# Kernel optimization log

Measured on AMD Instinct MI355X. Metric: run time of the kernel, lower is better.

Reference implementation:

```python
import jax, jax.numpy as jnp
import numpy as np

P = 0.1  # channel error probability (init kwarg error_prob)


def _binary_entropy(p):
    # matches tensor_binary_entropy: clamp log2 at dtype min
    q = 1.0 - p
    min_real = jnp.finfo(jnp.float32).min
    l2p = jnp.maximum(jnp.log2(p), min_real)
    l2q = jnp.maximum(jnp.log2(q), min_real)
    return -p * l2p - q * l2q


def setup_inputs() -> dict:
    key = jax.random.key(0)
    k1, k2, k3, k4 = jax.random.split(key, 4)
    B, L, V = 128, 64, 4096
    logits = jax.random.normal(k1, (B, L, V), jnp.float32)
    probs = jax.nn.softmax(logits, axis=-1)          # relaxed one-hot probs
    entropy = jax.random.uniform(k2, (B, L), jnp.float32)
    rand_mask = jax.random.uniform(k3, (B, L), jnp.float32)
    replacement_ids = jax.random.randint(k4, (B, L), 0, V - 2)
    return {"probs": probs, "entropy": entropy,
            "rand_mask": rand_mask, "replacement_ids": replacement_ids}


def reference(probs, entropy, rand_mask, replacement_ids):
    # SymmetricChannel.gs, training branch, fully vectorized / predicated.
    B, L, V = probs.shape
    mask = rand_mask < P                                  # [B,L] target positions
    any_hit = mask.any()                                  # torch early-returns if sum()==0

    # torch: replaced_probs[:, replacement_symbols] = 1 - eos  -> every masked row
    # is written at EVERY column appearing among the masked replacement ids.
    col_hit = jnp.zeros((V,), bool).at[replacement_ids.reshape(-1)].max(mask.reshape(-1))

    eos = probs[..., :1]                                  # [B,L,1] original EOS prob
    col = jnp.arange(V)
    base = jnp.where(col == 0, eos, jnp.zeros_like(eos))  # replaced_probs[:,0]=eos
    replaced = jnp.where(col_hit, 1.0 - eos, base)        # [B,L,V]

    probs_out = jnp.where(mask[..., None] & any_hit, replaced, probs)

    # torch adds H_b(p) + log2(probs.size(1) - 2)  (size(1) == max_len, kept faithfully)
    delta = _binary_entropy(jnp.float32(P)) + jnp.log2(jnp.float32(L - 2))
    entropy_out = jnp.where(any_hit, entropy + delta, entropy)
    return probs_out, entropy_out
```

## Files before the change

### kernel.cpp

```cpp
#include <hip/hip_runtime.h>


#define V_DIM   4096
#define N_ROWS  8192
#define P_CONST 0.1f
#define DELTA_CONST 6.4231919039761563f

typedef float f32x4 __attribute__((ext_vector_type(4)));

__global__ __launch_bounds__(256)
void sc_fused_kernel(const f32x4* __restrict__ probs4,
                     const float* __restrict__ probs_s,
                     const f32x4* __restrict__ rand4,
                     const float* __restrict__ rand_s,
                     const int*   __restrict__ repl,
                     const float* __restrict__ entropy,
                     f32x4*       __restrict__ out4,
                     float*       __restrict__ entropy_out)
{
    __shared__ unsigned colhit[V_DIM / 32];
    __shared__ unsigned anyflag;
    const int t   = threadIdx.x;
    const int bid = blockIdx.x;

    if (bid < N_ROWS) {
        const int  row      = bid;
        const long rowbase4 = (long)row * (V_DIM / 4);
        const bool m        = rand_s[row] < P_CONST;

        if (m) {
            if (t < V_DIM / 32) colhit[t] = 0u;
            __syncthreads();
            #pragma unroll
            for (int k = 0; k < N_ROWS / 4 / 256; ++k) {
                const int   i4 = t + k * 256;
                const f32x4 r  = rand4[i4];
                const int   i0 = i4 * 4;
                if (r.x < P_CONST) { const int id = repl[i0    ]; atomicOr(&colhit[id >> 5], 1u << (id & 31)); }
                if (r.y < P_CONST) { const int id = repl[i0 + 1]; atomicOr(&colhit[id >> 5], 1u << (id & 31)); }
                if (r.z < P_CONST) { const int id = repl[i0 + 2]; atomicOr(&colhit[id >> 5], 1u << (id & 31)); }
                if (r.w < P_CONST) { const int id = repl[i0 + 3]; atomicOr(&colhit[id >> 5], 1u << (id & 31)); }
            }
            __syncthreads();

            const float eos = probs_s[(long)row * V_DIM];
            const float om  = 1.0f - eos;
            #pragma unroll
            for (int k = 0; k < 4; ++k) {
                const int      c4 = t + k * 256;
                const unsigned w  = colhit[c4 >> 3];
                const int      c0 = c4 * 4;
                f32x4 r;
                r.x = ((w >> ( c0      & 31)) & 1u) ? om : ((c0 == 0) ? eos : 0.0f);
                r.y = ((w >> ((c0 + 1) & 31)) & 1u) ? om : 0.0f;
                r.z = ((w >> ((c0 + 2) & 31)) & 1u) ? om : 0.0f;
                r.w = ((w >> ((c0 + 3) & 31)) & 1u) ? om : 0.0f;
                __builtin_nontemporal_store(r, &out4[rowbase4 + c4]);
            }
        } else {
            #pragma unroll
            for (int k = 0; k < 4; ++k) {
                const int   c4 = t + k * 256;
                const f32x4 v  = __builtin_nontemporal_load(&probs4[rowbase4 + c4]);
                __builtin_nontemporal_store(v, &out4[rowbase4 + c4]);
            }
        }
    } else {
        const int eb = bid - N_ROWS;
        if (t == 0) anyflag = 0u;
        __syncthreads();
        bool la = false;
        #pragma unroll
        for (int k = 0; k < N_ROWS / 4 / 256; ++k) {
            const f32x4 r = rand4[t + k * 256];
            la = la || (r.x < P_CONST) || (r.y < P_CONST) ||
                       (r.z < P_CONST) || (r.w < P_CONST);
        }
        if (la) atomicOr(&anyflag, 1u);
        __syncthreads();
        const float d = anyflag ? DELTA_CONST : 0.0f;
        const int   i = eb * 256 + t;
        entropy_out[i] = entropy[i] + d;
    }
}

extern "C" void kernel_launch(void* const* d_in, const int* in_sizes, int n_in,
                              void* d_out, int out_size, void* d_ws, size_t ws_size,
                              hipStream_t stream)
{
    const float* probs     = (const float*)d_in[0];
    const float* entropy   = (const float*)d_in[1];
    const float* rand_mask = (const float*)d_in[2];
    const int*   repl      = (const int*)  d_in[3];

    float* out         = (float*)d_out;
    float* probs_out   = out;
    float* entropy_out = out + (long)N_ROWS * V_DIM;

    sc_fused_kernel<<<N_ROWS + 32, 256, 0, stream>>>(
        (const f32x4*)probs, probs,
        (const f32x4*)rand_mask, rand_mask,
        repl, entropy,
        (f32x4*)probs_out, entropy_out);
}
```

Measured before the change: 50.39 us.

## Hoist column-hit bitmap into single-block prefix kernel, process two rows per block

Adds a single-block prefix kernel that builds the column-hit bitmap and the any-hit flag once, writes the bitmap to workspace, and updates entropy. Before, every masked row's block rescanned all 8192 mask/replacement entries. The main kernel then processes two rows per block and copies the small bitmap from global memory only when a row is masked. This removes the redundant per-row scans in exchange for a second kernel launch and a serial dependency on a tiny one-block kernel.

```diff
diff --git a/kernel.cpp b/kernel.cpp
--- a/kernel.cpp
+++ b/kernel.cpp
@@ -2,85 +2,116 @@
 
 
 #define V_DIM   4096
+#define V4      (V_DIM / 4)
 #define N_ROWS  8192
 #define P_CONST 0.1f
 #define DELTA_CONST 6.4231919039761563f
 
 typedef float f32x4 __attribute__((ext_vector_type(4)));
 
-__global__ __launch_bounds__(256)
-void sc_fused_kernel(const f32x4* __restrict__ probs4,
-                     const float* __restrict__ probs_s,
-                     const f32x4* __restrict__ rand4,
-                     const float* __restrict__ rand_s,
-                     const int*   __restrict__ repl,
-                     const float* __restrict__ entropy,
-                     f32x4*       __restrict__ out4,
-                     float*       __restrict__ entropy_out)
+__global__ __launch_bounds__(1024)
+void sc_prefix_kernel(const f32x4* __restrict__ rand4,
+                      const int4*  __restrict__ repl4,
+                      const f32x4* __restrict__ entropy4,
+                      unsigned*    __restrict__ colhit_out,
+                      f32x4*       __restrict__ entropy_out4)
 {
     __shared__ unsigned colhit[V_DIM / 32];
     __shared__ unsigned anyflag;
-    const int t   = threadIdx.x;
-    const int bid = blockIdx.x;
+    const int t = threadIdx.x;
+    if (t < V_DIM / 32) colhit[t] = 0u;
+    if (t == 0) anyflag = 0u;
+    __syncthreads();
 
-    if (bid < N_ROWS) {
-        const int  row      = bid;
-        const long rowbase4 = (long)row * (V_DIM / 4);
-        const bool m        = rand_s[row] < P_CONST;
+    const f32x4 r0 = rand4[t], r1 = rand4[t + 1024];
+    const int4  q0 = repl4[t], q1 = repl4[t + 1024];
 
-        if (m) {
-            if (t < V_DIM / 32) colhit[t] = 0u;
-            __syncthreads();
-            #pragma unroll
-            for (int k = 0; k < N_ROWS / 4 / 256; ++k) {
-                const int   i4 = t + k * 256;
-                const f32x4 r  = rand4[i4];
-                const int   i0 = i4 * 4;
-                if (r.x < P_CONST) { const int id = repl[i0    ]; atomicOr(&colhit[id >> 5], 1u << (id & 31)); }
-                if (r.y < P_CONST) { const int id = repl[i0 + 1]; atomicOr(&colhit[id >> 5], 1u << (id & 31)); }
-                if (r.z < P_CONST) { const int id = repl[i0 + 2]; atomicOr(&colhit[id >> 5], 1u << (id & 31)); }
-                if (r.w < P_CONST) { const int id = repl[i0 + 3]; atomicOr(&colhit[id >> 5], 1u << (id & 31)); }
-            }
-            __syncthreads();
+    bool any = false;
+    {
+        if (r0.x < P_CONST) { any = true; atomicOr(&colhit[q0.x >> 5], 1u << (q0.x & 31)); }
+        if (r0.y < P_CONST) { any = true; atomicOr(&colhit[q0.y >> 5], 1u << (q0.y & 31)); }
+        if (r0.z < P_CONST) { any = true; atomicOr(&colhit[q0.z >> 5], 1u << (q0.z & 31)); }
+        if (r0.w < P_CONST) { any = true; atomicOr(&colhit[q0.w >> 5], 1u << (q0.w & 31)); }
+        if (r1.x < P_CONST) { any = true; atomicOr(&colhit[q1.x >> 5], 1u << (q1.x & 31)); }
+        if (r1.y < P_CONST) { any = true; atomicOr(&colhit[q1.y >> 5], 1u << (q1.y & 31)); }
+        if (r1.z < P_CONST) { any = true; atomicOr(&colhit[q1.z >> 5], 1u << (q1.z & 31)); }
+        if (r1.w < P_CONST) { any = true; atomicOr(&colhit[q1.w >> 5], 1u << (q1.w & 31)); }
+    }
+    if (any) atomicOr(&anyflag, 1u);
+    __syncthreads();
 
-            const float eos = probs_s[(long)row * V_DIM];
-            const float om  = 1.0f - eos;
-            #pragma unroll
-            for (int k = 0; k < 4; ++k) {
-                const int      c4 = t + k * 256;
-                const unsigned w  = colhit[c4 >> 3];
-                const int      c0 = c4 * 4;
-                f32x4 r;
-                r.x = ((w >> ( c0      & 31)) & 1u) ? om : ((c0 == 0) ? eos : 0.0f);
-                r.y = ((w >> ((c0 + 1) & 31)) & 1u) ? om : 0.0f;
-                r.z = ((w >> ((c0 + 2) & 31)) & 1u) ? om : 0.0f;
-                r.w = ((w >> ((c0 + 3) & 31)) & 1u) ? om : 0.0f;
-                __builtin_nontemporal_store(r, &out4[rowbase4 + c4]);
-            }
-        } else {
-            #pragma unroll
-            for (int k = 0; k < 4; ++k) {
-                const int   c4 = t + k * 256;
-                const f32x4 v  = __builtin_nontemporal_load(&probs4[rowbase4 + c4]);
-                __builtin_nontemporal_store(v, &out4[rowbase4 + c4]);
-            }
+    if (t < V_DIM / 32) colhit_out[t] = colhit[t];
+
+    const float d = anyflag ? DELTA_CONST : 0.0f;
+    f32x4 e0 = entropy4[t], e1 = entropy4[t + 1024];
+    e0.x += d; e0.y += d; e0.z += d; e0.w += d;
+    e1.x += d; e1.y += d; e1.z += d; e1.w += d;
+    entropy_out4[t]        = e0;
+    entropy_out4[t + 1024] = e1;
+}
+
+__device__ __forceinline__ void synth_row(const unsigned* colhit, float eos,
+                                          long rowbase4, int t,
+                                          f32x4* __restrict__ out4)
+{
+    const float om = 1.0f - eos;
+    #pragma unroll
+    for (int k = 0; k < 4; ++k) {
+        const int      c4 = t + k * 256;
+        const unsigned w  = colhit[c4 >> 3];
+        const int      c0 = c4 * 4;
+        f32x4 r;
+        r.x = ((w >> ( c0      & 31)) & 1u) ? om : ((c0 == 0) ? eos : 0.0f);
+        r.y = ((w >> ((c0 + 1) & 31)) & 1u) ? om : 0.0f;
+        r.z = ((w >> ((c0 + 2) & 31)) & 1u) ? om : 0.0f;
+        r.w = ((w >> ((c0 + 3) & 31)) & 1u) ? om : 0.0f;
+        __builtin_nontemporal_store(r, &out4[rowbase4 + c4]);
+    }
+}
+
+__global__ __launch_bounds__(256)
+void sc_main_kernel(const f32x4*    __restrict__ probs4,
+                    const float*    __restrict__ probs_s,
+                    const float*    __restrict__ rand_s,
+                    const unsigned* __restrict__ colhit_g,
+                    f32x4*          __restrict__ out4)
+{
+    __shared__ unsigned colhit[V_DIM / 32];
+    const int  t     = threadIdx.x;
+    const int  row0  = blockIdx.x * 2;
+    const bool m0    = rand_s[row0]     < P_CONST;
+    const bool m1    = rand_s[row0 + 1] < P_CONST;
+    const long base4 = (long)row0 * V4;
+
+    if (!m0 && !m1) {
+        #pragma unroll
+        for (int k = 0; k < 8; ++k) {
+            const f32x4 v = probs4[base4 + t + k * 256];
+            __builtin_nontemporal_store(v, &out4[base4 + t + k * 256]);
         }
+        return;
+    }
+
+    if (t < V_DIM / 32) colhit[t] = colhit_g[t];
+    __syncthreads();
+
+    if (m0) {
+        synth_row(colhit, probs_s[(long)row0 * V_DIM], base4, t, out4);
     } else {
-        const int eb = bid - N_ROWS;
-        if (t == 0) anyflag = 0u;
-        __syncthreads();
-        bool la = false;
         #pragma unroll
-        for (int k = 0; k < N_ROWS / 4 / 256; ++k) {
-            const f32x4 r = rand4[t + k * 256];
-            la = la || (r.x < P_CONST) || (r.y < P_CONST) ||
-                       (r.z < P_CONST) || (r.w < P_CONST);
+        for (int k = 0; k < 4; ++k) {
+            const f32x4 v = probs4[base4 + t + k * 256];
+            __builtin_nontemporal_store(v, &out4[base4 + t + k * 256]);
         }
-        if (la) atomicOr(&anyflag, 1u);
-        __syncthreads();
-        const float d = anyflag ? DELTA_CONST : 0.0f;
-        const int   i = eb * 256 + t;
-        entropy_out[i] = entropy[i] + d;
+    }
+    if (m1) {
+        synth_row(colhit, probs_s[(long)(row0 + 1) * V_DIM], base4 + V4, t, out4);
+    } else {
+        #pragma unroll
+        for (int k = 0; k < 4; ++k) {
+            const f32x4 v = probs4[base4 + V4 + t + k * 256];
+            __builtin_nontemporal_store(v, &out4[base4 + V4 + t + k * 256]);
+        }
     }
 }
 
@@ -93,13 +124,15 @@
     const float* rand_mask = (const float*)d_in[2];
     const int*   repl      = (const int*)  d_in[3];
 
-    float* out         = (float*)d_out;
-    float* probs_out   = out;
-    float* entropy_out = out + (long)N_ROWS * V_DIM;
+    float*    out         = (float*)d_out;
+    float*    probs_out   = out;
+    float*    entropy_out = out + (long)N_ROWS * V_DIM;
+    unsigned* colhit_ws   = (unsigned*)d_ws;
 
-    sc_fused_kernel<<<N_ROWS + 32, 256, 0, stream>>>(
-        (const f32x4*)probs, probs,
-        (const f32x4*)rand_mask, rand_mask,
-        repl, entropy,
-        (f32x4*)probs_out, entropy_out);
+    sc_prefix_kernel<<<1, 1024, 0, stream>>>(
+        (const f32x4*)rand_mask, (const int4*)repl,
+        (const f32x4*)entropy, colhit_ws, (f32x4*)entropy_out);
+
+    sc_main_kernel<<<N_ROWS / 2, 256, 0, stream>>>(
+        (const f32x4*)probs, probs, rand_mask, colhit_ws, (f32x4*)probs_out);
 }
```

Result: faster. 47.55 us (-5.6%).

## Build column bitmap once per writer block and split copy from synthesis

Applied to the files above, without the earlier changes.

Before, every masked row's block rebuilt the full column-hit bitmap by scanning all 8192 mask entries. Now 256 dedicated writer blocks each build the bitmap once and synthesize the masked rows in their 32-row slice. The entropy update is folded into those same writer blocks. Copy blocks now handle two rows each and only copy unmasked rows, with vectorized int4 loads of the replacement ids. The trade-off is that writer blocks loop serially over their rows, which can cause load imbalance.

```diff
diff --git a/kernel.cpp b/kernel.cpp
--- a/kernel.cpp
+++ b/kernel.cpp
@@ -2,85 +2,106 @@
 
 
 #define V_DIM   4096
+#define V4      (V_DIM / 4)
 #define N_ROWS  8192
+#define NWRITER 256
+#define WROWS   (N_ROWS / NWRITER)
 #define P_CONST 0.1f
 #define DELTA_CONST 6.4231919039761563f
 
 typedef float f32x4 __attribute__((ext_vector_type(4)));
 
+__device__ __forceinline__ void synth_row(const unsigned* colhit, float eos,
+                                          long rowbase4, int t,
+                                          f32x4* __restrict__ out4)
+{
+    const float om = 1.0f - eos;
+    #pragma unroll
+    for (int k = 0; k < 4; ++k) {
+        const int      c4 = t + k * 256;
+        const unsigned w  = colhit[c4 >> 3];
+        const int      c0 = c4 * 4;
+        f32x4 r;
+        r.x = ((w >> ( c0      & 31)) & 1u) ? om : ((c0 == 0) ? eos : 0.0f);
+        r.y = ((w >> ((c0 + 1) & 31)) & 1u) ? om : 0.0f;
+        r.z = ((w >> ((c0 + 2) & 31)) & 1u) ? om : 0.0f;
+        r.w = ((w >> ((c0 + 3) & 31)) & 1u) ? om : 0.0f;
+        __builtin_nontemporal_store(r, &out4[rowbase4 + c4]);
+    }
+}
+
 __global__ __launch_bounds__(256)
-void sc_fused_kernel(const f32x4* __restrict__ probs4,
-                     const float* __restrict__ probs_s,
-                     const f32x4* __restrict__ rand4,
-                     const float* __restrict__ rand_s,
-                     const int*   __restrict__ repl,
-                     const float* __restrict__ entropy,
-                     f32x4*       __restrict__ out4,
-                     float*       __restrict__ entropy_out)
+void sc_onekernel(const f32x4* __restrict__ probs4,
+                  const float* __restrict__ probs_s,
+                  const f32x4* __restrict__ rand4,
+                  const float* __restrict__ rand_s,
+                  const int4*  __restrict__ repl4,
+                  const float* __restrict__ entropy,
+                  f32x4*       __restrict__ out4,
+                  float*       __restrict__ entropy_out)
 {
-    __shared__ unsigned colhit[V_DIM / 32];
-    __shared__ unsigned anyflag;
     const int t   = threadIdx.x;
     const int bid = blockIdx.x;
 
-    if (bid < N_ROWS) {
-        const int  row      = bid;
-        const long rowbase4 = (long)row * (V_DIM / 4);
-        const bool m        = rand_s[row] < P_CONST;
+    if (bid < NWRITER) {
+        __shared__ unsigned colhit[V_DIM / 32];
+        __shared__ unsigned anyflag;
+        if (t < V_DIM / 32) colhit[t] = 0u;
+        if (t == 0) anyflag = 0u;
+        __syncthreads();
 
-        if (m) {
-            if (t < V_DIM / 32) colhit[t] = 0u;
-            __syncthreads();
-            #pragma unroll
-            for (int k = 0; k < N_ROWS / 4 / 256; ++k) {
-                const int   i4 = t + k * 256;
-                const f32x4 r  = rand4[i4];
-                const int   i0 = i4 * 4;
-                if (r.x < P_CONST) { const int id = repl[i0    ]; atomicOr(&colhit[id >> 5], 1u << (id & 31)); }
-                if (r.y < P_CONST) { const int id = repl[i0 + 1]; atomicOr(&colhit[id >> 5], 1u << (id & 31)); }
-                if (r.z < P_CONST) { const int id = repl[i0 + 2]; atomicOr(&colhit[id >> 5], 1u << (id & 31)); }
-                if (r.w < P_CONST) { const int id = repl[i0 + 3]; atomicOr(&colhit[id >> 5], 1u << (id & 31)); }
-            }
-            __syncthreads();
+        bool any = false;
+        #pragma unroll
+        for (int k = 0; k < N_ROWS / 4 / 256; ++k) {
+            const int   i4 = t + k * 256;
+            const f32x4 r  = rand4[i4];
+            const int4  q  = repl4[i4];
+            if (r.x < P_CONST) { any = true; atomicOr(&colhit[q.x >> 5], 1u << (q.x & 31)); }
+            if (r.y < P_CONST) { any = true; atomicOr(&colhit[q.y >> 5], 1u << (q.y & 31)); }
+            if (r.z < P_CONST) { any = true; atomicOr(&colhit[q.z >> 5], 1u << (q.z & 31)); }
+            if (r.w < P_CONST) { any = true; atomicOr(&colhit[q.w >> 5], 1u << (q.w & 31)); }
+        }
+        if (any) atomicOr(&anyflag, 1u);
+        __syncthreads();
 
-            const float eos = probs_s[(long)row * V_DIM];
-            const float om  = 1.0f - eos;
-            #pragma unroll
-            for (int k = 0; k < 4; ++k) {
-                const int      c4 = t + k * 256;
-                const unsigned w  = colhit[c4 >> 3];
-                const int      c0 = c4 * 4;
-                f32x4 r;
-                r.x = ((w >> ( c0      & 31)) & 1u) ? om : ((c0 == 0) ? eos : 0.0f);
-                r.y = ((w >> ((c0 + 1) & 31)) & 1u) ? om : 0.0f;
-                r.z = ((w >> ((c0 + 2) & 31)) & 1u) ? om : 0.0f;
-                r.w = ((w >> ((c0 + 3) & 31)) & 1u) ? om : 0.0f;
-                __builtin_nontemporal_store(r, &out4[rowbase4 + c4]);
-            }
-        } else {
-            #pragma unroll
-            for (int k = 0; k < 4; ++k) {
-                const int   c4 = t + k * 256;
-                const f32x4 v  = __builtin_nontemporal_load(&probs4[rowbase4 + c4]);
-                __builtin_nontemporal_store(v, &out4[rowbase4 + c4]);
+        const float d  = anyflag ? DELTA_CONST : 0.0f;
+        const int   e0 = bid * WROWS;
+        if (t < WROWS) entropy_out[e0 + t] = entropy[e0 + t] + d;
+
+        for (int r = e0; r < e0 + WROWS; ++r) {
+            if (rand_s[r] < P_CONST) {
+                synth_row(colhit, probs_s[(long)r * V_DIM],
+                          (long)r * V4, t, out4);
             }
         }
     } else {
-        const int eb = bid - N_ROWS;
-        if (t == 0) anyflag = 0u;
-        __syncthreads();
-        bool la = false;
-        #pragma unroll
-        for (int k = 0; k < N_ROWS / 4 / 256; ++k) {
-            const f32x4 r = rand4[t + k * 256];
-            la = la || (r.x < P_CONST) || (r.y < P_CONST) ||
-                       (r.z < P_CONST) || (r.w < P_CONST);
+        const int  r0    = (bid - NWRITER) * 2;
+        const bool m0    = rand_s[r0]     < P_CONST;
+        const bool m1    = rand_s[r0 + 1] < P_CONST;
+        const long base4 = (long)r0 * V4;
+
+        if (!m0 && !m1) {
+            #pragma unroll
+            for (int k = 0; k < 8; ++k) {
+                const f32x4 v = probs4[base4 + t + k * 256];
+                __builtin_nontemporal_store(v, &out4[base4 + t + k * 256]);
+            }
+            return;
         }
-        if (la) atomicOr(&anyflag, 1u);
-        __syncthreads();
-        const float d = anyflag ? DELTA_CONST : 0.0f;
-        const int   i = eb * 256 + t;
-        entropy_out[i] = entropy[i] + d;
+        if (!m0) {
+            #pragma unroll
+            for (int k = 0; k < 4; ++k) {
+                const f32x4 v = probs4[base4 + t + k * 256];
+                __builtin_nontemporal_store(v, &out4[base4 + t + k * 256]);
+            }
+        }
+        if (!m1) {
+            #pragma unroll
+            for (int k = 0; k < 4; ++k) {
+                const f32x4 v = probs4[base4 + V4 + t + k * 256];
+                __builtin_nontemporal_store(v, &out4[base4 + V4 + t + k * 256]);
+            }
+        }
     }
 }
 
@@ -97,9 +118,9 @@
     float* probs_out   = out;
     float* entropy_out = out + (long)N_ROWS * V_DIM;
 
-    sc_fused_kernel<<<N_ROWS + 32, 256, 0, stream>>>(
+    sc_onekernel<<<NWRITER + N_ROWS / 2, 256, 0, stream>>>(
         (const f32x4*)probs, probs,
         (const f32x4*)rand_mask, rand_mask,
-        repl, entropy,
+        (const int4*)repl, entropy,
         (f32x4*)probs_out, entropy_out);
 }
```

Measured after the change: 42.71 us. 15.2% less time.
